# Kernel tuning notes

Hardware: AMD Instinct MI355X
Metric: run time of the kernel (lower is better)

## Reference

```python
import math
import jax, jax.numpy as jnp
import numpy as np

N_HEAD = 16
ROPE_BASE = 10000.0


def _rope_tables(T, half, dtype):
    # build_sin_cos(seq_len, dim=head_dim//2): inv freq of length `half`
    pos = jnp.arange(T, dtype=jnp.float32)[:, None]                       # (T,1)
    inv = jnp.exp(jnp.arange(0, 2 * half, 2, dtype=jnp.float32) * (-math.log(ROPE_BASE) / (2 * half)))
    ang = pos * inv                                                        # (T, half)
    return jnp.sin(ang).astype(dtype), jnp.cos(ang).astype(dtype)


def _apply_rope(q, k, sin, cos):
    # q,k: (B,T,H,Dh); sin,cos: (T, Dh//2) -> broadcast over batch and heads
    half = q.shape[-1] // 2
    s = sin[None, :, None, :]
    c = cos[None, :, None, :]
    q1, q2 = q[..., :half], q[..., half:]
    k1, k2 = k[..., :half], k[..., half:]
    q = jnp.concatenate([q1 * c - q2 * s, q2 * c + q1 * s], axis=-1)
    k = jnp.concatenate([k1 * c - k2 * s, k2 * c + k1 * s], axis=-1)
    return q, k


def setup_inputs() -> dict:
    key = jax.random.key(0)
    k1, k2, k3 = jax.random.split(key, 3)
    B, T, C = 2, 2048, 2048
    x = jax.random.normal(k1, (B, T, C), dtype=jnp.float32)
    w_qkv = jax.random.normal(k2, (3 * C, C), dtype=jnp.float32) * (1.0 / math.sqrt(C))
    w_proj = jax.random.normal(k3, (C, C), dtype=jnp.float32) * (1.0 / math.sqrt(C))
    return {"x": x, "w_qkv": w_qkv, "w_proj": w_proj}


def reference(x, w_qkv, w_proj):
    B, T, C = x.shape
    H = N_HEAD
    Dh = C // H
    # fused QKV projection (Linear, no bias): (B,T,3C) -> (B,T,3,H,Dh)
    qkv = jnp.einsum('btc,oc->bto', x, w_qkv).reshape(B, T, 3, H, Dh)
    q, k, v = qkv[:, :, 0], qkv[:, :, 1], qkv[:, :, 2]          # (B,T,H,Dh)
    sin, cos = _rope_tables(T, Dh // 2, x.dtype)
    q, k = _apply_rope(q, k, sin, cos)
    # causal attention, scale 1/sqrt(Dh) (flash default softmax_scale=None)
    scale = 1.0 / math.sqrt(Dh)
    scores = jnp.einsum('bqhd,bkhd->bhqk', q, k) * scale        # (B,H,T,T)
    mask = jnp.tril(jnp.ones((T, T), dtype=bool))
    scores = jnp.where(mask[None, None], scores, jnp.finfo(scores.dtype).min)
    probs = jax.nn.softmax(scores, axis=-1)
    out = jnp.einsum('bhqk,bkhd->bqhd', probs, v)               # (B,T,H,Dh)
    # faithful to original: permute(0,2,1,3) then reshape_as(x)
    out = jnp.transpose(out, (0, 2, 1, 3)).reshape(B, T, C)
    return jnp.einsum('btc,oc->bto', out, w_proj)
```

## Files before the change

### kernel.cpp

```cpp
#include <hip/hip_runtime.h>
#include <hip/hip_bf16.h>

typedef __bf16 bf16_t;
typedef __bf16 bf16x8 __attribute__((ext_vector_type(8)));
typedef float f32x4 __attribute__((ext_vector_type(4)));

#define MFMA16(a, b, c) __builtin_amdgcn_mfma_f32_16x16x32_bf16(a, b, c, 0, 0, 0)

__device__ __forceinline__ void async_copy16(const void* g, void* l) {
  __builtin_amdgcn_global_load_lds(
      (const __attribute__((address_space(1))) void*)g,
      (__attribute__((address_space(3))) void*)l, 16, 0, 0);
}

__global__ void cast_f32_bf16(const float* __restrict__ in, bf16_t* __restrict__ out, int n8) {
  int stride = gridDim.x * blockDim.x;
  for (int i = blockIdx.x * blockDim.x + threadIdx.x; i < n8; i += stride) {
    const float* p = in + (size_t)i * 8;
    f32x4 a = *(const f32x4*)p;
    f32x4 b = *(const f32x4*)(p + 4);
    bf16x8 o;
    o[0] = (bf16_t)a[0]; o[1] = (bf16_t)a[1]; o[2] = (bf16_t)a[2]; o[3] = (bf16_t)a[3];
    o[4] = (bf16_t)b[0]; o[5] = (bf16_t)b[1]; o[6] = (bf16_t)b[2]; o[7] = (bf16_t)b[3];
    *(bf16x8*)(out + (size_t)i * 8) = o;
  }
}

__global__ __launch_bounds__(512, 2) void gemm_qkv(
    const bf16_t* __restrict__ A, const bf16_t* __restrict__ Bw,
    bf16_t* __restrict__ qo, bf16_t* __restrict__ ko, bf16_t* __restrict__ vto,
    int K) {
  __shared__ __align__(16) char lds[131072];
  int tid = threadIdx.x;
  int w = tid >> 6, lane = tid & 63;
  int wm = w & 1, wn = w >> 1;
  int mr = lane & 15, kg = lane >> 4;

  int orig = blockIdx.x;
  int chunk = orig & 7, i = orig >> 3;
  int by = (chunk & 3) * 4 + (i & 3);
  int bx = (chunk >> 2) * 12 + (i >> 2);
  int row0 = by * 256, col0 = bx * 256;

  int lr = tid >> 3, ch = (tid & 7) ^ (lr & 7);
  size_t aoff[4], boff[4];
#pragma unroll
  for (int g = 0; g < 4; ++g) {
    int gr = g * 32 + (lr & 31) + (lr >> 5) * 128;
    aoff[g] = (size_t)(row0 + gr) * K + ch * 8;
  }
#pragma unroll
  for (int p = 0; p < 4; ++p) {
    int gr = (lr >> 4) * 64 + p * 16 + (lr & 15);
    boff[p] = (size_t)(col0 + gr) * K + ch * 8;
  }

  auto stgA = [&](int q, int g, int kt) {
    async_copy16(A + aoff[g] + kt * 64, lds + q * 65536 + g * 8192 + tid * 16);
  };
  auto stgB = [&](int q, int p, int kt) {
    async_copy16(Bw + boff[p] + kt * 64, lds + q * 65536 + 32768 + p * 8192 + tid * 16);
  };

  f32x4 zero = {0.f, 0.f, 0.f, 0.f};
  f32x4 acc[8][4];
#pragma unroll
  for (int mi = 0; mi < 8; ++mi)
#pragma unroll
    for (int ni = 0; ni < 4; ++ni) acc[mi][ni] = zero;

  int nt = K >> 6;

  stgB(0, 0, 0); stgB(0, 1, 0); stgB(0, 2, 0); stgB(0, 3, 0);
  stgA(0, 0, 0); stgA(0, 1, 0); stgA(0, 2, 0); stgA(0, 3, 0);
  asm volatile("s_waitcnt vmcnt(0)" ::: "memory");
  __builtin_amdgcn_sched_barrier(0);
  __builtin_amdgcn_s_barrier();
  __builtin_amdgcn_sched_barrier(0);

#pragma unroll 1
  for (int t = 0; t < nt; ++t) {
    int q = t & 1, qn = q ^ 1;
    int kt = (t + 1 < nt) ? (t + 1) : t;
    const char* Ab = lds + q * 65536;
    const char* Bb = Ab + 32768;
    bf16x8 bf[4][2];

#define QKV_PHASE(MI0, STG0, STG1, WAIT)                                        \
    {                                                                           \
      int r0 = ((MI0) >> 1) * 64 + wm * 32 + mr;                                \
      int r1 = r0 + 16;                                                         \
      bf16x8 a00 = *(const bf16x8*)(Ab + r0 * 128 + ((kg * 16) ^ ((r0 & 7) << 4)));      \
      bf16x8 a01 = *(const bf16x8*)(Ab + r0 * 128 + ((64 + kg * 16) ^ ((r0 & 7) << 4))); \
      bf16x8 a10 = *(const bf16x8*)(Ab + r1 * 128 + ((kg * 16) ^ ((r1 & 7) << 4)));      \
      bf16x8 a11 = *(const bf16x8*)(Ab + r1 * 128 + ((64 + kg * 16) ^ ((r1 & 7) << 4))); \
      STG0; STG1;                                                               \
      __builtin_amdgcn_sched_barrier(0);                                        \
      asm volatile("s_waitcnt vmcnt(" #WAIT ")" ::: "memory");                  \
      __builtin_amdgcn_s_barrier();                                             \
      asm volatile("s_waitcnt lgkmcnt(0)" ::: "memory");                        \
      __builtin_amdgcn_sched_barrier(0);                                        \
      __builtin_amdgcn_s_setprio(1);                                            \
      _Pragma("unroll")                                                         \
      for (int ni = 0; ni < 4; ++ni) {                                          \
        acc[MI0][ni] = MFMA16(a00, bf[ni][0], acc[MI0][ni]);                    \
        acc[MI0][ni] = MFMA16(a01, bf[ni][1], acc[MI0][ni]);                    \
        acc[(MI0) + 1][ni] = MFMA16(a10, bf[ni][0], acc[(MI0) + 1][ni]);        \
        acc[(MI0) + 1][ni] = MFMA16(a11, bf[ni][1], acc[(MI0) + 1][ni]);        \
      }                                                                         \
      __builtin_amdgcn_s_setprio(0);                                            \
      __builtin_amdgcn_sched_barrier(0);                                        \
      __builtin_amdgcn_s_barrier();                                             \
      __builtin_amdgcn_sched_barrier(0);                                        \
    }

#pragma unroll
    for (int ni = 0; ni < 4; ++ni) {
      int rb = ni * 64 + wn * 16 + mr;
      bf[ni][0] = *(const bf16x8*)(Bb + rb * 128 + ((kg * 16) ^ ((rb & 7) << 4)));
      bf[ni][1] = *(const bf16x8*)(Bb + rb * 128 + ((64 + kg * 16) ^ ((rb & 7) << 4)));
    }
    QKV_PHASE(0, stgB(qn, 0, kt), stgB(qn, 1, kt), 4)
    QKV_PHASE(2, stgB(qn, 2, kt), stgB(qn, 3, kt), 5)
    QKV_PHASE(4, stgA(qn, 0, kt), stgA(qn, 1, kt), 6)
    QKV_PHASE(6, stgA(qn, 2, kt), stgA(qn, 3, kt), 3)
#undef QKV_PHASE
  }
  asm volatile("s_waitcnt vmcnt(0)" ::: "memory");
  __syncthreads();

  char* tb = &lds[0];
  int s = col0 >> 11;
  int h0 = (col0 >> 7) & 15;
  int b = row0 >> 11, t0 = row0 & 2047;
  if (s < 2) {
#pragma unroll
    for (int mi = 0; mi < 8; ++mi)
#pragma unroll
      for (int ni = 0; ni < 4; ++ni)
#pragma unroll
        for (int jj = 0; jj < 4; ++jj) {
          int rl = wm * 128 + mi * 16 + kg * 4 + jj;
          int cb = (wn * 64 + ni * 16 + mr) * 2;
          *(bf16_t*)(tb + rl * 512 + (cb ^ ((rl & 7) << 4))) = (bf16_t)acc[mi][ni][jj];
        }
    __syncthreads();
    int r = tid >> 1, hs = tid & 1;
    const char* rowb = tb + r * 512;
    int sz = (r & 7) << 4;
    int t = t0 + r;
    bf16_t* dst = (s == 0 ? qo : ko) + ((size_t)((b * 16 + h0 + hs) * 2048 + t)) * 128;
    float tf = (float)t;
    const float cinv = -0.20762050593046014f;
    bf16x8 vin[16];
#pragma unroll
    for (int m = 0; m < 16; ++m)
      vin[m] = *(const bf16x8*)(rowb + ((hs * 256 + m * 16) ^ sz));
#pragma unroll
    for (int m = 0; m < 8; ++m) {
      bf16x8 o1, o2;
#pragma unroll
      for (int e = 0; e < 8; ++e) {
        float ang = tf * exp2f((float)(m * 8 + e) * cinv);
        float sv = __sinf(ang), cv = __cosf(ang);
        float x1 = (float)vin[m][e], x2 = (float)vin[m + 8][e];
        o1[e] = (bf16_t)(x1 * cv - x2 * sv);
        o2[e] = (bf16_t)(x2 * cv + x1 * sv);
      }
      *(bf16x8*)(dst + m * 8) = o1;
      *(bf16x8*)(dst + 64 + m * 8) = o2;
    }
  } else {
#pragma unroll
    for (int mi = 0; mi < 8; ++mi)
#pragma unroll
      for (int ni = 0; ni < 4; ++ni)
#pragma unroll
        for (int jj = 0; jj < 4; ++jj) {
          int rl = wm * 128 + mi * 16 + kg * 4 + jj;
          int cl = wn * 64 + ni * 16 + mr;
          *(bf16_t*)(tb + cl * 512 + ((rl * 2) ^ ((cl & 7) << 4))) = (bf16_t)acc[mi][ni][jj];
        }
    __syncthreads();
    int d = tid >> 1, ts = tid & 1;
    const char* rowb = tb + d * 512;
    int sz = (d & 7) << 4;
    bf16_t* dst = vto + ((size_t)((b * 16 + h0 + (d >> 7)) * 128 + (d & 127))) * 2048 +
                  t0 + ts * 128;
#pragma unroll
    for (int m = 0; m < 16; ++m)
      *(bf16x8*)(dst + m * 8) = *(const bf16x8*)(rowb + ((ts * 256 + m * 16) ^ sz));
  }
}

__global__ __launch_bounds__(512, 2) void gemm256(
    const bf16_t* __restrict__ A, const bf16_t* __restrict__ Bw, float* __restrict__ C,
    int M, int N, int K, int nby) {
  __shared__ __align__(16) char lds[147456];
  int tid = threadIdx.x;
  int w = tid >> 6, lane = tid & 63;
  int wm = w >> 1, wn = w & 1;
  int mr = lane & 15, kg = lane >> 4;

  int nwg = gridDim.x;
  int orig = blockIdx.x;
  int wgid = (orig & 7) * (nwg >> 3) + (orig >> 3);
  int by = wgid % nby, bx = wgid / nby;
  int row0 = by * 256, col0 = bx * 128;

  size_t aoff[4], boff[2];
#pragma unroll
  for (int it = 0; it < 4; ++it) {
    int c = tid + it * 512;
    int r = c >> 3;
    int chs = (c & 7) ^ (r & 7);
    aoff[it] = (size_t)(row0 + r) * K + chs * 8;
  }
#pragma unroll
  for (int it = 0; it < 2; ++it) {
    int c = tid + it * 512;
    int r = c >> 3;
    int chs = (c & 7) ^ (r & 7);
    boff[it] = (size_t)(col0 + r) * K + chs * 8;
  }

  auto stageA = [&](int buf, int kt, int half) {
    char* Ad = &lds[buf * 49152];
#pragma unroll
    for (int it = half * 2; it < half * 2 + 2; ++it)
      async_copy16(A + aoff[it] + kt * 64, Ad + (tid + it * 512) * 16);
  };
  auto stageB = [&](int buf, int kt) {
    char* Bd = &lds[buf * 49152 + 32768];
#pragma unroll
    for (int it = 0; it < 2; ++it)
      async_copy16(Bw + boff[it] + kt * 64, Bd + (tid + it * 512) * 16);
  };

  f32x4 zero = {0.f, 0.f, 0.f, 0.f};
  f32x4 acc[4][4];
#pragma unroll
  for (int mi = 0; mi < 4; ++mi)
#pragma unroll
    for (int ni = 0; ni < 4; ++ni) acc[mi][ni] = zero;

  int nt = K >> 6;
  stageA(0, 0, 0); stageA(0, 0, 1); stageB(0, 0);
  stageA(1, 1, 0); stageA(1, 1, 1); stageB(1, 1);
  asm volatile("s_waitcnt vmcnt(6)" ::: "memory");
  __builtin_amdgcn_sched_barrier(0);
  __builtin_amdgcn_s_barrier();
  __builtin_amdgcn_sched_barrier(0);

#pragma unroll 1
  for (int t = 0; t < nt; ++t) {
    int cur = t % 3;
    int nxt = (t + 2) % 3;
    int kt2 = (t + 2 < nt) ? (t + 2) : t;
    const char* Ab = &lds[cur * 49152];
    const char* Bb = &lds[cur * 49152 + 32768];
    bf16x8 af[4][2], bfr[4][2];
#pragma unroll
    for (int mi = 0; mi < 4; ++mi) {
      int row = wm * 64 + mi * 16 + mr;
      const char* rb = Ab + row * 128;
      int sz = (row & 7) << 4;
      af[mi][0] = *(const bf16x8*)(rb + ((kg * 16) ^ sz));
      af[mi][1] = *(const bf16x8*)(rb + ((64 + kg * 16) ^ sz));
    }
#pragma unroll
    for (int ni = 0; ni < 4; ++ni) {
      int row = wn * 64 + ni * 16 + mr;
      const char* rb = Bb + row * 128;
      int sz = (row & 7) << 4;
      bfr[ni][0] = *(const bf16x8*)(rb + ((kg * 16) ^ sz));
      bfr[ni][1] = *(const bf16x8*)(rb + ((64 + kg * 16) ^ sz));
    }
    stageA(nxt, kt2, 0);
    __builtin_amdgcn_s_setprio(1);
#pragma unroll
    for (int mi = 0; mi < 4; ++mi) {
      acc[mi][0] = MFMA16(af[mi][0], bfr[0][0], acc[mi][0]);
      acc[mi][0] = MFMA16(af[mi][1], bfr[0][1], acc[mi][0]);
    }
    __builtin_amdgcn_s_setprio(0);
    stageA(nxt, kt2, 1);
    __builtin_amdgcn_s_setprio(1);
#pragma unroll
    for (int mi = 0; mi < 4; ++mi) {
      acc[mi][1] = MFMA16(af[mi][0], bfr[1][0], acc[mi][1]);
      acc[mi][1] = MFMA16(af[mi][1], bfr[1][1], acc[mi][1]);
    }
    __builtin_amdgcn_s_setprio(0);
    stageB(nxt, kt2);
    __builtin_amdgcn_s_setprio(1);
#pragma unroll
    for (int mi = 0; mi < 4; ++mi) {
      acc[mi][2] = MFMA16(af[mi][0], bfr[2][0], acc[mi][2]);
      acc[mi][2] = MFMA16(af[mi][1], bfr[2][1], acc[mi][2]);
      acc[mi][3] = MFMA16(af[mi][0], bfr[3][0], acc[mi][3]);
      acc[mi][3] = MFMA16(af[mi][1], bfr[3][1], acc[mi][3]);
    }
    __builtin_amdgcn_s_setprio(0);
    asm volatile("s_waitcnt vmcnt(6)" ::: "memory");
    __builtin_amdgcn_sched_barrier(0);
    __builtin_amdgcn_s_barrier();
    __builtin_amdgcn_sched_barrier(0);
  }
  asm volatile("s_waitcnt vmcnt(0)" ::: "memory");
  __syncthreads();

#pragma unroll
  for (int mi = 0; mi < 4; ++mi)
#pragma unroll
    for (int ni = 0; ni < 4; ++ni)
#pragma unroll
      for (int jj = 0; jj < 4; ++jj) {
        int row = row0 + wm * 64 + mi * 16 + kg * 4 + jj;
        int col = col0 + wn * 64 + ni * 16 + mr;
        C[(size_t)row * N + col] = acc[mi][ni][jj];
      }
}

__global__ __launch_bounds__(256) void attn_kernel(
    const bf16_t* __restrict__ qg, const bf16_t* __restrict__ kgl,
    const bf16_t* __restrict__ vtg, bf16_t* __restrict__ og) {
  __shared__ __align__(16) bf16_t Ks[2][64 * 128];
  __shared__ __align__(16) bf16_t Vs[2][128 * 64];
  __shared__ __align__(16) bf16_t plds[4][1024];
  const int T = 2048;
  int tid = threadIdx.x;
  int w = tid >> 6, lane = tid & 63;
  int mr = lane & 15, kg = lane >> 4;
  int swz = (mr & 7) << 4;

  int L = blockIdx.y * 16 + blockIdx.x;
  int role = (L & 7) * 64 + (L >> 3);
  int bx = role & 15, bh = role >> 4;

  const bf16_t* Q = qg + (size_t)bh * T * 128;
  const bf16_t* K = kgl + (size_t)bh * T * 128;
  const bf16_t* Vt = vtg + (size_t)bh * 128 * T;

  int sb = tid * 16;
  int krl = sb >> 8;
  int kc = (sb & 255) ^ ((krl & 7) << 4);
  size_t ksrc = (size_t)krl * 128 + (kc >> 1);
  int vdl = sb >> 7;
  int vc = (sb & 127) ^ ((vdl & 7) << 4);
  size_t vsrc = (size_t)vdl * 2048 + (vc >> 1);

  auto stage = [&](int buf, int kb) {
#pragma unroll
    for (int it = 0; it < 4; ++it)
      async_copy16(K + (size_t)(kb + it * 16) * 128 + ksrc, &Ks[buf][it * 2048 + tid * 8]);
#pragma unroll
    for (int it = 0; it < 4; ++it)
      async_copy16(Vt + (size_t)it * 65536 + kb + vsrc, &Vs[buf][it * 2048 + tid * 8]);
  };

  const float cscale = 0.12751744f;
  f32x4 zero = {0.f, 0.f, 0.f, 0.f};
  bf16_t* P = &plds[w][0];
  int b = bh >> 4, h = bh & 15;

#pragma unroll 1
  for (int ph = 0; ph < 2; ++ph) {
    int qb = ph ? bx : (31 - bx);
    int qr0 = qb * 64 + w * 16;
    bf16x8 qf[4];
#pragma unroll
    for (int db = 0; db < 4; ++db)
      qf[db] = *(const bf16x8*)(Q + (size_t)(qr0 + mr) * 128 + db * 32 + kg * 8);

    f32x4 acc[8];
#pragma unroll
    for (int d2 = 0; d2 < 8; ++d2) acc[d2] = zero;
    float mrun[4] = {-1e30f, -1e30f, -1e30f, -1e30f};
    float lrun[4] = {0.f, 0.f, 0.f, 0.f};

    int nj = qb + 1;
    __syncthreads();
    stage(0, 0);
    int cur = 0;
#pragma unroll 1
    for (int j = 0; j < nj; ++j) {
      __syncthreads();
      if (j + 1 < nj) stage(cur ^ 1, (j + 1) * 64);
      const char* KsB = (const char*)&Ks[cur][0];
      const char* VsB = (const char*)&Vs[cur][0];
      int kb = j * 64;
      f32x4 s[4];
#pragma unroll
      for (int ntl = 0; ntl < 4; ++ntl) {
        s[ntl] = zero;
        int rowb = (ntl * 16 + mr) * 256;
#pragma unroll
        for (int db = 0; db < 4; ++db) {
          bf16x8 kf = *(const bf16x8*)(KsB + rowb + ((db * 64 + kg * 16) ^ swz));
          s[ntl] = MFMA16(qf[db], kf, s[ntl]);
        }
      }
      float pvv[4][4];
      float tmax[4] = {-3e38f, -3e38f, -3e38f, -3e38f};
      bool diag = (j == qb);
#pragma unroll
      for (int ntl = 0; ntl < 4; ++ntl)
#pragma unroll
        for (int jj = 0; jj < 4; ++jj) {
          float v = s[ntl][jj] * cscale;
          if (diag && (kb + ntl * 16 + mr) > (qr0 + kg * 4 + jj)) v = -1e30f;
          pvv[ntl][jj] = v;
          tmax[jj] = fmaxf(tmax[jj], v);
        }
#pragma unroll
      for (int m = 1; m < 16; m <<= 1)
#pragma unroll
        for (int jj = 0; jj < 4; ++jj)
          tmax[jj] = fmaxf(tmax[jj], __shfl_xor(tmax[jj], m, 64));
      bool ok = true;
#pragma unroll
      for (int jj = 0; jj < 4; ++jj) ok &= (tmax[jj] <= mrun[jj] + 8.0f);
      if (!__all(ok)) {
#pragma unroll
        for (int jj = 0; jj < 4; ++jj) {
          float mn = fmaxf(mrun[jj], tmax[jj]);
          float corr = __builtin_amdgcn_exp2f(mrun[jj] - mn);
          mrun[jj] = mn;
          lrun[jj] *= corr;
#pragma unroll
          for (int d2 = 0; d2 < 8; ++d2) acc[d2][jj] *= corr;
        }
      }
      float rs[4] = {0.f, 0.f, 0.f, 0.f};
#pragma unroll
      for (int ntl = 0; ntl < 4; ++ntl)
#pragma unroll
        for (int jj = 0; jj < 4; ++jj) {
          float p = __builtin_amdgcn_exp2f(pvv[ntl][jj] - mrun[jj]);
          pvv[ntl][jj] = p;
          rs[jj] += p;
        }
#pragma unroll
      for (int m = 1; m < 16; m <<= 1)
#pragma unroll
        for (int jj = 0; jj < 4; ++jj) rs[jj] += __shfl_xor(rs[jj], m, 64);
#pragma unroll
      for (int jj = 0; jj < 4; ++jj) lrun[jj] += rs[jj];
#pragma unroll
      for (int ntl = 0; ntl < 4; ++ntl)
#pragma unroll
        for (int jj = 0; jj < 4; ++jj) {
          int rr = kg * 4 + jj;
          int cbyte = (mr + ntl * 16) * 2;
          *(bf16_t*)((char*)P + rr * 128 + (cbyte ^ ((rr & 7) << 4))) = (bf16_t)pvv[ntl][jj];
        }
#pragma unroll
      for (int ks = 0; ks < 2; ++ks) {
        int cb = (ks * 32 + kg * 8) * 2;
        bf16x8 pa = *(const bf16x8*)((const char*)P + mr * 128 + (cb ^ ((mr & 7) << 4)));
#pragma unroll
        for (int d2 = 0; d2 < 8; ++d2) {
          bf16x8 vf = *(const bf16x8*)(VsB + (d2 * 16 + mr) * 128 + ((ks * 64 + kg * 16) ^ swz));
          acc[d2] = MFMA16(pa, vf, acc[d2]);
        }
      }
      cur ^= 1;
    }
#pragma unroll
    for (int jj = 0; jj < 4; ++jj) {
      float invl = 1.0f / lrun[jj];
      int t = qr0 + kg * 4 + jj;
      size_t row = (size_t)b * 2048 + h * 128 + (t >> 4);
      bf16_t* orow = og + row * 2048 + (t & 15) * 128;
#pragma unroll
      for (int d2 = 0; d2 < 8; ++d2)
        orow[d2 * 16 + mr] = (bf16_t)(acc[d2][jj] * invl);
    }
  }
}

extern "C" void kernel_launch(void* const* d_in, const int* in_sizes, int n_in,
                              void* d_out, int out_size, void* d_ws, size_t ws_size,
                              hipStream_t stream) {
  const float* x = (const float*)d_in[0];
  const float* wqkv = (const float*)d_in[1];
  const float* wproj = (const float*)d_in[2];
  float* out = (float*)d_out;
  char* ws = (char*)d_ws;

  const size_t OFF_WQKV = 16777216;
  const size_t OFF_Q = 41943040;
  const size_t OFF_K = 58720256;
  const size_t OFF_VT = 75497472;

  bf16_t* xb = (bf16_t*)(ws);
  bf16_t* wqkvb = (bf16_t*)(ws + OFF_WQKV);
  bf16_t* g_q = (bf16_t*)(ws + OFF_Q);
  bf16_t* g_k = (bf16_t*)(ws + OFF_K);
  bf16_t* g_vt = (bf16_t*)(ws + OFF_VT);
  bf16_t* g_att = (bf16_t*)(ws);
  bf16_t* wprojb = (bf16_t*)(ws + OFF_WQKV);

  cast_f32_bf16<<<2048, 256, 0, stream>>>(x, xb, 8388608 / 8);
  cast_f32_bf16<<<2048, 256, 0, stream>>>(wqkv, wqkvb, 12582912 / 8);
  gemm_qkv<<<384, 512, 0, stream>>>(xb, wqkvb, g_q, g_k, g_vt, 2048);
  cast_f32_bf16<<<2048, 256, 0, stream>>>(wproj, wprojb, 4194304 / 8);
  attn_kernel<<<dim3(16, 32), 256, 0, stream>>>(g_q, g_k, g_vt, g_att);
  gemm256<<<256, 512, 0, stream>>>(g_att, wprojb, out, 4096, 2048, 2048, 16);
}
```

Baseline: 276.5 us.

## Split V projection into separate 256x128 GEMM launch and raise MFMA priority in attention

```diff
diff --git a/kernel.cpp b/kernel.cpp
--- a/kernel.cpp
+++ b/kernel.cpp
@@ -28,7 +28,7 @@
 
 __global__ __launch_bounds__(512, 2) void gemm_qkv(
     const bf16_t* __restrict__ A, const bf16_t* __restrict__ Bw,
-    bf16_t* __restrict__ qo, bf16_t* __restrict__ ko, bf16_t* __restrict__ vto,
+    bf16_t* __restrict__ qo, bf16_t* __restrict__ ko,
     int K) {
   __shared__ __align__(16) char lds[131072];
   int tid = threadIdx.x;
@@ -39,7 +39,7 @@
   int orig = blockIdx.x;
   int chunk = orig & 7, i = orig >> 3;
   int by = (chunk & 3) * 4 + (i & 3);
-  int bx = (chunk >> 2) * 12 + (i >> 2);
+  int bx = (chunk >> 2) * 8 + (i >> 2);
   int row0 = by * 256, col0 = bx * 256;
 
   int lr = tid >> 3, ch = (tid & 7) ^ (lr & 7);
@@ -133,69 +133,48 @@
   int s = col0 >> 11;
   int h0 = (col0 >> 7) & 15;
   int b = row0 >> 11, t0 = row0 & 2047;
-  if (s < 2) {
-#pragma unroll
-    for (int mi = 0; mi < 8; ++mi)
-#pragma unroll
-      for (int ni = 0; ni < 4; ++ni)
-#pragma unroll
-        for (int jj = 0; jj < 4; ++jj) {
-          int rl = wm * 128 + mi * 16 + kg * 4 + jj;
-          int cb = (wn * 64 + ni * 16 + mr) * 2;
-          *(bf16_t*)(tb + rl * 512 + (cb ^ ((rl & 7) << 4))) = (bf16_t)acc[mi][ni][jj];
-        }
-    __syncthreads();
-    int r = tid >> 1, hs = tid & 1;
-    const char* rowb = tb + r * 512;
-    int sz = (r & 7) << 4;
-    int t = t0 + r;
-    bf16_t* dst = (s == 0 ? qo : ko) + ((size_t)((b * 16 + h0 + hs) * 2048 + t)) * 128;
-    float tf = (float)t;
-    const float cinv = -0.20762050593046014f;
-    bf16x8 vin[16];
-#pragma unroll
-    for (int m = 0; m < 16; ++m)
-      vin[m] = *(const bf16x8*)(rowb + ((hs * 256 + m * 16) ^ sz));
-#pragma unroll
-    for (int m = 0; m < 8; ++m) {
-      bf16x8 o1, o2;
-#pragma unroll
-      for (int e = 0; e < 8; ++e) {
-        float ang = tf * exp2f((float)(m * 8 + e) * cinv);
-        float sv = __sinf(ang), cv = __cosf(ang);
-        float x1 = (float)vin[m][e], x2 = (float)vin[m + 8][e];
-        o1[e] = (bf16_t)(x1 * cv - x2 * sv);
-        o2[e] = (bf16_t)(x2 * cv + x1 * sv);
+#pragma unroll
+  for (int mi = 0; mi < 8; ++mi)
+#pragma unroll
+    for (int ni = 0; ni < 4; ++ni)
+#pragma unroll
+      for (int jj = 0; jj < 4; ++jj) {
+        int rl = wm * 128 + mi * 16 + kg * 4 + jj;
+        int cb = (wn * 64 + ni * 16 + mr) * 2;
+        *(bf16_t*)(tb + rl * 512 + (cb ^ ((rl & 7) << 4))) = (bf16_t)acc[mi][ni][jj];
       }
-      *(bf16x8*)(dst + m * 8) = o1;
-      *(bf16x8*)(dst + 64 + m * 8) = o2;
-    }
-  } else {
-#pragma unroll
-    for (int mi = 0; mi < 8; ++mi)
-#pragma unroll
-      for (int ni = 0; ni < 4; ++ni)
-#pragma unroll
-        for (int jj = 0; jj < 4; ++jj) {
-          int rl = wm * 128 + mi * 16 + kg * 4 + jj;
-          int cl = wn * 64 + ni * 16 + mr;
-          *(bf16_t*)(tb + cl * 512 + ((rl * 2) ^ ((cl & 7) << 4))) = (bf16_t)acc[mi][ni][jj];
-        }
-    __syncthreads();
-    int d = tid >> 1, ts = tid & 1;
-    const char* rowb = tb + d * 512;
-    int sz = (d & 7) << 4;
-    bf16_t* dst = vto + ((size_t)((b * 16 + h0 + (d >> 7)) * 128 + (d & 127))) * 2048 +
-                  t0 + ts * 128;
-#pragma unroll
-    for (int m = 0; m < 16; ++m)
-      *(bf16x8*)(dst + m * 8) = *(const bf16x8*)(rowb + ((ts * 256 + m * 16) ^ sz));
+  __syncthreads();
+  int r = tid >> 1, hs = tid & 1;
+  const char* rowb = tb + r * 512;
+  int sz = (r & 7) << 4;
+  int t = t0 + r;
+  bf16_t* dst = (s == 0 ? qo : ko) + ((size_t)((b * 16 + h0 + hs) * 2048 + t)) * 128;
+  float tf = (float)t;
+  const float cinv = -0.20762050593046014f;
+  bf16x8 vin[16];
+#pragma unroll
+  for (int m = 0; m < 16; ++m)
+    vin[m] = *(const bf16x8*)(rowb + ((hs * 256 + m * 16) ^ sz));
+#pragma unroll
+  for (int m = 0; m < 8; ++m) {
+    bf16x8 o1, o2;
+#pragma unroll
+    for (int e = 0; e < 8; ++e) {
+      float ang = tf * exp2f((float)(m * 8 + e) * cinv);
+      float sv = __sinf(ang), cv = __cosf(ang);
+      float x1 = (float)vin[m][e], x2 = (float)vin[m + 8][e];
+      o1[e] = (bf16_t)(x1 * cv - x2 * sv);
+      o2[e] = (bf16_t)(x2 * cv + x1 * sv);
+    }
+    *(bf16x8*)(dst + m * 8) = o1;
+    *(bf16x8*)(dst + 64 + m * 8) = o2;
   }
 }
 
+template <int MODE>
 __global__ __launch_bounds__(512, 2) void gemm256(
     const bf16_t* __restrict__ A, const bf16_t* __restrict__ Bw, float* __restrict__ C,
-    int M, int N, int K, int nby) {
+    bf16_t* __restrict__ vto, int M, int N, int K, int nby, int colbase) {
   __shared__ __align__(16) char lds[147456];
   int tid = threadIdx.x;
   int w = tid >> 6, lane = tid & 63;
@@ -206,7 +185,7 @@
   int orig = blockIdx.x;
   int wgid = (orig & 7) * (nwg >> 3) + (orig >> 3);
   int by = wgid % nby, bx = wgid / nby;
-  int row0 = by * 256, col0 = bx * 128;
+  int row0 = by * 256, col0 = colbase + bx * 128;
 
   size_t aoff[4], boff[2];
 #pragma unroll
@@ -221,7 +200,7 @@
     int c = tid + it * 512;
     int r = c >> 3;
     int chs = (c & 7) ^ (r & 7);
-    boff[it] = (size_t)(col0 + r) * K + chs * 8;
+    boff[it] = (size_t)(col0 - colbase + r) * K + chs * 8;
   }
 
   auto stageA = [&](int buf, int kt, int half) {
@@ -310,16 +289,41 @@
   asm volatile("s_waitcnt vmcnt(0)" ::: "memory");
   __syncthreads();
 
-#pragma unroll
-  for (int mi = 0; mi < 4; ++mi)
-#pragma unroll
-    for (int ni = 0; ni < 4; ++ni)
-#pragma unroll
-      for (int jj = 0; jj < 4; ++jj) {
-        int row = row0 + wm * 64 + mi * 16 + kg * 4 + jj;
-        int col = col0 + wn * 64 + ni * 16 + mr;
-        C[(size_t)row * N + col] = acc[mi][ni][jj];
-      }
+  if (MODE == 0) {
+#pragma unroll
+    for (int mi = 0; mi < 4; ++mi)
+#pragma unroll
+      for (int ni = 0; ni < 4; ++ni)
+#pragma unroll
+        for (int jj = 0; jj < 4; ++jj) {
+          int row = row0 + wm * 64 + mi * 16 + kg * 4 + jj;
+          int col = col0 + wn * 64 + ni * 16 + mr;
+          C[(size_t)row * N + col] = acc[mi][ni][jj];
+        }
+  } else {
+    char* tb = &lds[0];
+    int h = (col0 >> 7) & 15;
+    int b = row0 >> 11, t0 = row0 & 2047;
+#pragma unroll
+    for (int mi = 0; mi < 4; ++mi)
+#pragma unroll
+      for (int ni = 0; ni < 4; ++ni)
+#pragma unroll
+        for (int jj = 0; jj < 4; ++jj) {
+          int rloc = wm * 64 + mi * 16 + kg * 4 + jj;
+          int cloc = wn * 64 + ni * 16 + mr;
+          *(bf16_t*)(tb + cloc * 512 + ((rloc * 2) ^ ((cloc & 7) << 4))) =
+              (bf16_t)acc[mi][ni][jj];
+        }
+    __syncthreads();
+    int d = tid >> 2, qt = tid & 3;
+    const char* rowb = tb + d * 512;
+    int sz = (d & 7) << 4;
+    bf16_t* dst = vto + ((size_t)((b * 16 + h) * 128 + d)) * 2048 + t0 + qt * 64;
+#pragma unroll
+    for (int m2 = 0; m2 < 8; ++m2)
+      *(bf16x8*)(dst + m2 * 8) = *(const bf16x8*)(rowb + ((qt * 128 + m2 * 16) ^ sz));
+  }
 }
 
 __global__ __launch_bounds__(256) void attn_kernel(
@@ -391,6 +395,7 @@
       const char* VsB = (const char*)&Vs[cur][0];
       int kb = j * 64;
       f32x4 s[4];
+      __builtin_amdgcn_s_setprio(1);
 #pragma unroll
       for (int ntl = 0; ntl < 4; ++ntl) {
         s[ntl] = zero;
@@ -401,6 +406,7 @@
           s[ntl] = MFMA16(qf[db], kf, s[ntl]);
         }
       }
+      __builtin_amdgcn_s_setprio(0);
       float pvv[4][4];
       float tmax[4] = {-3e38f, -3e38f, -3e38f, -3e38f};
       bool diag = (j == qb);
@@ -455,6 +461,7 @@
           int cbyte = (mr + ntl * 16) * 2;
           *(bf16_t*)((char*)P + rr * 128 + (cbyte ^ ((rr & 7) << 4))) = (bf16_t)pvv[ntl][jj];
         }
+      __builtin_amdgcn_s_setprio(1);
 #pragma unroll
       for (int ks = 0; ks < 2; ++ks) {
         int cb = (ks * 32 + kg * 8) * 2;
@@ -465,6 +472,7 @@
           acc[d2] = MFMA16(pa, vf, acc[d2]);
         }
       }
+      __builtin_amdgcn_s_setprio(0);
       cur ^= 1;
     }
 #pragma unroll
@@ -504,8 +512,10 @@
 
   cast_f32_bf16<<<2048, 256, 0, stream>>>(x, xb, 8388608 / 8);
   cast_f32_bf16<<<2048, 256, 0, stream>>>(wqkv, wqkvb, 12582912 / 8);
-  gemm_qkv<<<384, 512, 0, stream>>>(xb, wqkvb, g_q, g_k, g_vt, 2048);
+  gemm_qkv<<<256, 512, 0, stream>>>(xb, wqkvb, g_q, g_k, 2048);
+  gemm256<1><<<256, 512, 0, stream>>>(xb, wqkvb + (size_t)4096 * 2048, nullptr, g_vt,
+                                      4096, 2048, 2048, 16, 4096);
   cast_f32_bf16<<<2048, 256, 0, stream>>>(wproj, wprojb, 4194304 / 8);
   attn_kernel<<<dim3(16, 32), 256, 0, stream>>>(g_q, g_k, g_vt, g_att);
-  gemm256<<<256, 512, 0, stream>>>(g_att, wprojb, out, 4096, 2048, 2048, 16);
+  gemm256<0><<<256, 512, 0, stream>>>(g_att, wprojb, out, nullptr, 4096, 2048, 2048, 16, 0);
 }
```

After: 267.1 us. 1.04x faster.
